# Kernel optimization log

Measured on AMD Instinct MI355X. Metric: run time of the kernel, lower is better.

The kernel has to match this reference:

```python
import jax, jax.numpy as jnp
import numpy as np

N = 200000
E = 6400000


def setup_inputs() -> dict:
    key = jax.random.key(0)
    k1, k2, k3, k4 = jax.random.split(key, 4)
    x = jax.random.normal(k1, (N, 10), dtype=jnp.float32)
    edge_index = jax.random.randint(k2, (2, E), 0, N, dtype=jnp.int64)
    W1 = jax.random.normal(k3, (10, 16), dtype=jnp.float32) * (1.0 / np.sqrt(10))
    b1 = jnp.zeros((16,), dtype=jnp.float32)
    W2 = jax.random.normal(k4, (16, 2), dtype=jnp.float32) * (1.0 / np.sqrt(16))
    b2 = jnp.zeros((2,), dtype=jnp.float32)
    return {"x": x, "edge_index": edge_index, "W1": W1, "b1": b1, "W2": W2, "b2": b2}


def gcn_layer(x, src, dst, W, b, num_nodes):
    # GCNConv: out = D^{-1/2} (A + I) D^{-1/2} (x W) + b, deg computed on A+I
    loop = jnp.arange(num_nodes, dtype=src.dtype)
    s = jnp.concatenate([src, loop])
    d = jnp.concatenate([dst, loop])
    deg = jax.ops.segment_sum(jnp.ones(s.shape[0], dtype=x.dtype), d, num_segments=num_nodes)
    dinv = jnp.where(deg > 0, jax.lax.rsqrt(deg), 0.0)
    norm = dinv[s] * dinv[d]                      # [E+N]
    h = x @ W                                     # [N, out] (transform before gather)
    msg = h[s] * norm[:, None]                    # [E+N, out]
    return jax.ops.segment_sum(msg, d, num_segments=num_nodes) + b


def reference(x, edge_index, W1, b1, W2, b2):
    src, dst = edge_index[0], edge_index[1]
    n = x.shape[0]
    h = jax.nn.relu(gcn_layer(x, src, dst, W1, b1, n))
    return gcn_layer(h, src, dst, W2, b2, n)
```

## Files before the change

### kernel.cpp

```cpp
#include <hip/hip_runtime.h>
#include <hip/hip_fp16.h>

#define BLK 256
#define BBLK 512
#define ABLK 512
#define DBLK 512
#define NBK 782
#define BW 256
#define NK2 512
#define NPAD (NBK * BW)
#define HALF (NPAD / 2)
#define CAP 8960
#define NCH 3
#define CHUNK 6144


__global__ void k_hist(const int* __restrict__ dst, int e, int* __restrict__ gcnt,
                       int* __restrict__ blockhist) {
  __shared__ int h[NBK];
  for (int i = threadIdx.x; i < NBK; i += BLK) h[i] = 0;
  __syncthreads();
  int base = blockIdx.x * CHUNK;
  int m = min(CHUNK, e - base);
  int m4 = m >> 2;
  const int4* d4 = (const int4*)(dst + base);
  for (int k = threadIdx.x; k < m4; k += BLK) {
    int4 vv = d4[k];
    atomicAdd(&h[vv.x >> 8], 1);
    atomicAdd(&h[vv.y >> 8], 1);
    atomicAdd(&h[vv.z >> 8], 1);
    atomicAdd(&h[vv.w >> 8], 1);
  }
  for (int k = (m4 << 2) + threadIdx.x; k < m; k += BLK)
    atomicAdd(&h[dst[base + k] >> 8], 1);
  __syncthreads();
  int* row = blockhist + (size_t)blockIdx.x * NBK;
  int sft = (blockIdx.x * 193) % NBK;
  for (int bb = threadIdx.x; bb < NBK; bb += BLK) {
    int b = bb + sft; if (b >= NBK) b -= NBK;
    int c = h[b];
    row[b] = c;
    if (c) atomicAdd(&gcnt[b], c);
  }
}

__global__ void k_scan(const int* __restrict__ gcnt, int* __restrict__ gbase,
                       int* __restrict__ gcur, int e) {
  __shared__ int s[1024];
  int t = threadIdx.x;
  int v = (t < NBK) ? gcnt[t] : 0;
  s[t] = v;
  __syncthreads();
  for (int d = 1; d < 1024; d <<= 1) {
    int u = (t >= d) ? s[t - d] : 0;
    __syncthreads();
    s[t] += u;
    __syncthreads();
  }
  if (t < NBK) { int ex = s[t] - v; gbase[t] = ex; gcur[t] = ex; }
  if (t == 0) gbase[NBK] = e;
}

__global__ void __launch_bounds__(BBLK) k_bin(const int* __restrict__ src,
                                              const int* __restrict__ dst, int e,
                                              int* __restrict__ gcur,
                                              const int* __restrict__ blockhist,
                                              unsigned* __restrict__ binned) {
  __shared__ int lcnt[NBK];
  __shared__ int loff[NBK + 1];
  __shared__ int lbase[NBK];
  __shared__ int part[BBLK];
  __shared__ unsigned sorted[CHUNK];
  __shared__ unsigned short bkt16[CHUNK];
  int t = threadIdx.x;
  int base = blockIdx.x * CHUNK;
  int m = min(CHUNK, e - base);

  const int* row = blockhist + (size_t)blockIdx.x * NBK;
  for (int i = t; i < NBK; i += BBLK) lcnt[i] = row[i];
  __syncthreads();
  int b0 = 2 * t;
  int s0 = (b0 + 0 < NBK) ? lcnt[b0 + 0] : 0;
  int s1 = (b0 + 1 < NBK) ? lcnt[b0 + 1] : 0;
  int tsum = s0 + s1;
  part[t] = tsum;
  __syncthreads();
  for (int d = 1; d < BBLK; d <<= 1) {
    int u = (t >= d) ? part[t - d] : 0;
    __syncthreads();
    part[t] += u;
    __syncthreads();
  }
  int ex = part[t] - tsum;
  if (b0 + 0 < NBK) loff[b0 + 0] = ex;
  if (b0 + 1 < NBK) loff[b0 + 1] = ex + s0;
  if (t == 0) loff[NBK] = m;
  __syncthreads();
  int sft = (blockIdx.x * 193) % NBK;
  for (int bb = t; bb < NBK; bb += BBLK) {
    int b = bb + sft; if (b >= NBK) b -= NBK;
    int c = lcnt[b];
    lbase[b] = c ? atomicAdd(&gcur[b], c) : 0;
  }
  __syncthreads();
  for (int b = t; b < NBK; b += BBLK) lcnt[b] = loff[b];
  __syncthreads();
  for (int k = t; k < m; k += BBLK) {
    int d = dst[base + k];
    int b = d >> 8;
    int dl = d & 255;
    int pos = atomicAdd(&lcnt[b], 1);
    sorted[pos] = (unsigned)src[base + k] | ((unsigned)dl << 18);
    bkt16[pos] = (unsigned short)b;
  }
  __syncthreads();
  for (int i = t; i < m; i += BBLK) {
    int b = bkt16[i];
    binned[lbase[b] + (i - loff[b])] = sorted[i];
  }
}

__global__ void __launch_bounds__(DBLK) k_ldeg_t1(const unsigned* __restrict__ binned,
                                                  const int* __restrict__ gbase,
                                                  const float* __restrict__ x,
                                                  const float* __restrict__ W1,
                                                  int* __restrict__ deg2,
                                                  float* __restrict__ dinv,
                                                  __half* __restrict__ hs1, int n) {
  __shared__ int cnt[2][NK2];
  __shared__ float w[160];
  int t = threadIdx.x;
  cnt[0][t] = 0;
  cnt[1][t] = 0;
  if (t < 160) w[t] = W1[t];
  __syncthreads();
  int b = blockIdx.x;
  int p0 = gbase[b], p1 = gbase[b + 1];
  int h = t >> 8;
#define KEYOF(u) ((int)(((u) >> 18) << 1) | (int)(((u) & 0x3FFFFu) >= HALF))
  int p = p0 + t;
  for (; p + 3 * DBLK < p1; p += 4 * DBLK) {
    unsigned u0 = binned[p];
    unsigned u1 = binned[p + DBLK];
    unsigned u2 = binned[p + 2 * DBLK];
    unsigned u3 = binned[p + 3 * DBLK];
    atomicAdd(&cnt[h][KEYOF(u0)], 1);
    atomicAdd(&cnt[h][KEYOF(u1)], 1);
    atomicAdd(&cnt[h][KEYOF(u2)], 1);
    atomicAdd(&cnt[h][KEYOF(u3)], 1);
  }
  for (; p < p1; p += DBLK) {
    unsigned u = binned[p];
    atomicAdd(&cnt[h][KEYOF(u)], 1);
  }
#undef KEYOF
  __syncthreads();
  deg2[(size_t)b * NK2 + t] = cnt[0][t] + cnt[1][t];
  if (t >= BW) return;
  int v = b * BW + t;
  if (v >= n) return;
  int dg = cnt[0][2 * t] + cnt[0][2 * t + 1] + cnt[1][2 * t] + cnt[1][2 * t + 1];
  float di = rsqrtf((float)dg + 1.0f);
  dinv[v] = di;
  float xi[10];
#pragma unroll
  for (int k = 0; k < 10; k++) xi[k] = x[(size_t)v * 10 + k];
  __half2 hv[8];
#pragma unroll
  for (int j = 0; j < 8; j++) {
    float acc0 = 0.f, acc1 = 0.f;
#pragma unroll
    for (int k = 0; k < 10; k++) {
      acc0 = fmaf(xi[k], w[k * 16 + 2 * j], acc0);
      acc1 = fmaf(xi[k], w[k * 16 + 2 * j + 1], acc1);
    }
    hv[j] = __floats2half2_rn(acc0 * di, acc1 * di);
  }
  float4* o = (float4*)(hs1 + (size_t)v * 16);
  o[0] = *(float4*)&hv[0];
  o[1] = *(float4*)&hv[4];
}

__global__ void __launch_bounds__(ABLK) k_agg1s(unsigned* __restrict__ binned,
                                                const int* __restrict__ gbase,
                                                const int* __restrict__ deg2,
                                                int* __restrict__ doff,
                                                const __half* __restrict__ hs1,
                                                const float* __restrict__ dinv,
                                                const float* __restrict__ b1,
                                                const float* __restrict__ W2,
                                                float* __restrict__ hs2, int n) {
  __shared__ int cnt[NK2];
  __shared__ int off[NK2 + 1];
  __shared__ int sorted[CAP];
  __shared__ float w2[32];
  __shared__ float sb1[16];
  int t = threadIdx.x;
  if (t < 32) w2[t] = W2[t];
  if (t >= 32 && t < 48) sb1[t - 32] = b1[t - 32];
  int bkt = blockIdx.x;
  int p0 = gbase[bkt], p1 = gbase[bkt + 1];
  const bool fast = (p1 - p0) <= CAP;
  const int j = t >> 1;
  const int c = t & 1;
  float acc[8];
#pragma unroll
  for (int q = 0; q < 8; q++) acc[q] = 0.f;

#define ACCR(R) { const __half2* h2_ = (const __half2*)&R; \
    float2 f0_ = __half22float2(h2_[0]); \
    float2 f1_ = __half22float2(h2_[1]); \
    float2 f2_ = __half22float2(h2_[2]); \
    float2 f3_ = __half22float2(h2_[3]); \
    acc[0] += f0_.x; acc[1] += f0_.y; acc[2] += f1_.x; acc[3] += f1_.y; \
    acc[4] += f2_.x; acc[5] += f2_.y; acc[6] += f3_.x; acc[7] += f3_.y; }

  int p = p0;
  int cidx = 0;
  while (p < p1) {
    int m = min(CAP, p1 - p);
    if (fast) {
      cnt[t] = deg2[(size_t)bkt * NK2 + t];
    } else {
      cnt[t] = 0;
      __syncthreads();
      for (int i = t; i < m; i += ABLK) {
        unsigned u = __builtin_nontemporal_load(&binned[p + i]);
        int key = (int)((u >> 18) << 1) | (int)((u & 0x3FFFFu) >= HALF);
        atomicAdd(&cnt[key], 1);
      }
    }
    __syncthreads();
    int myv = cnt[t];
    for (int d = 1; d < NK2; d <<= 1) {
      int u = (t >= d) ? cnt[t - d] : 0;
      __syncthreads();
      cnt[t] += u;
      __syncthreads();
    }
    off[t] = cnt[t] - myv;
    if (t == 0) off[NK2] = m;
    __syncthreads();
    cnt[t] = off[t];
    __syncthreads();
    for (int i = t; i < m; i += ABLK) {
      unsigned pk = __builtin_nontemporal_load(&binned[p + i]);
      int srcv = (int)(pk & 0x3FFFFu);
      int key = (int)((pk >> 18) << 1) | (int)(srcv >= HALF);
      int pos = atomicAdd(&cnt[key], 1);
      sorted[pos] = srcv;
    }
    __syncthreads();
    for (int i = t; i < m; i += ABLK)
      __builtin_nontemporal_store((unsigned)sorted[i], &binned[p + i]);
    if (cidx < NCH && t <= BW) doff[((size_t)bkt * NCH + cidx) * (BW + 1) + t] = off[2 * t];
    int iA0 = off[2 * j], iA1 = off[2 * j + 1], iB1 = off[2 * j + 2];
    int i = iA0;
    for (; i + 3 < iA1; i += 4) {
      int s0 = sorted[i + 0];
      int s1 = sorted[i + 1];
      int s2 = sorted[i + 2];
      int s3 = sorted[i + 3];
      float4 r0 = *(const float4*)(hs1 + (size_t)s0 * 16 + c * 8);
      float4 r1 = *(const float4*)(hs1 + (size_t)s1 * 16 + c * 8);
      float4 r2 = *(const float4*)(hs1 + (size_t)s2 * 16 + c * 8);
      float4 r3 = *(const float4*)(hs1 + (size_t)s3 * 16 + c * 8);
      ACCR(r0); ACCR(r1); ACCR(r2); ACCR(r3);
    }
    for (; i < iA1; i++) {
      float4 r = *(const float4*)(hs1 + (size_t)sorted[i] * 16 + c * 8);
      ACCR(r);
    }
    __syncthreads();
    for (; i + 3 < iB1; i += 4) {
      int s0 = sorted[i + 0];
      int s1 = sorted[i + 1];
      int s2 = sorted[i + 2];
      int s3 = sorted[i + 3];
      float4 r0 = *(const float4*)(hs1 + (size_t)s0 * 16 + c * 8);
      float4 r1 = *(const float4*)(hs1 + (size_t)s1 * 16 + c * 8);
      float4 r2 = *(const float4*)(hs1 + (size_t)s2 * 16 + c * 8);
      float4 r3 = *(const float4*)(hs1 + (size_t)s3 * 16 + c * 8);
      ACCR(r0); ACCR(r1); ACCR(r2); ACCR(r3);
    }
    for (; i < iB1; i++) {
      float4 r = *(const float4*)(hs1 + (size_t)sorted[i] * 16 + c * 8);
      ACCR(r);
    }
    __syncthreads();
    p += m;
    cidx++;
  }
#undef ACCR

  int v = bkt * BW + j;
  if (v < n) {
    float di = dinv[v];
    float4 sf = *(const float4*)(hs1 + (size_t)v * 16 + c * 8);
    const __half2* sh = (const __half2*)&sf;
    float h0c = 0.f, h1c = 0.f;
#pragma unroll
    for (int q = 0; q < 4; q++) {
      float2 sv = __half22float2(sh[q]);
      int f0 = c * 8 + 2 * q;
      int f1 = f0 + 1;
      float a0 = fmaxf(fmaf(di, acc[2 * q + 0] + sv.x, sb1[f0]), 0.f);
      float a1 = fmaxf(fmaf(di, acc[2 * q + 1] + sv.y, sb1[f1]), 0.f);
      h0c = fmaf(a0, w2[f0 * 2 + 0], fmaf(a1, w2[f1 * 2 + 0], h0c));
      h1c = fmaf(a0, w2[f0 * 2 + 1], fmaf(a1, w2[f1 * 2 + 1], h1c));
    }
    float h0 = h0c + __shfl_xor(h0c, 1);
    float h1 = h1c + __shfl_xor(h1c, 1);
    if (c == 0) {
      hs2[(size_t)v * 2 + 0] = h0 * di;
      hs2[(size_t)v * 2 + 1] = h1 * di;
    }
  }
}

__global__ void __launch_bounds__(BBLK) k_agg2(const unsigned* __restrict__ binned,
                                               const int* __restrict__ gbase,
                                               const int* __restrict__ doff,
                                               const float* __restrict__ hs2,
                                               const float* __restrict__ dinv,
                                               const float* __restrict__ b2,
                                               float* __restrict__ out, int n) {
  int t = threadIdx.x;
  int bkt = blockIdx.x >> 1;
  int j = (t >> 2) + ((blockIdx.x & 1) << 7);
  int c = t & 3;
  int p0 = gbase[bkt], p1 = gbase[bkt + 1];
  float a0 = 0.f, a1 = 0.f;
  int cidx = 0;
  for (int p = p0; p < p1; p += CAP, cidx++) {
    const int* row = doff + ((size_t)bkt * NCH + cidx) * (BW + 1);
    int i0 = row[j], i1 = row[j + 1];
    const unsigned* bp = binned + p;
    int i = i0 + c;
    for (; i + 12 < i1; i += 16) {
      int s0 = bp[i + 0];
      int s1 = bp[i + 4];
      int s2 = bp[i + 8];
      int s3 = bp[i + 12];
      float2 m0 = *(const float2*)(hs2 + (size_t)s0 * 2);
      float2 m1 = *(const float2*)(hs2 + (size_t)s1 * 2);
      float2 m2 = *(const float2*)(hs2 + (size_t)s2 * 2);
      float2 m3 = *(const float2*)(hs2 + (size_t)s3 * 2);
      a0 += m0.x + m1.x + m2.x + m3.x;
      a1 += m0.y + m1.y + m2.y + m3.y;
    }
    for (; i < i1; i += 4) {
      float2 m = *(const float2*)(hs2 + (size_t)bp[i] * 2);
      a0 += m.x;
      a1 += m.y;
    }
  }
  a0 += __shfl_xor(a0, 1);
  a0 += __shfl_xor(a0, 2);
  a1 += __shfl_xor(a1, 1);
  a1 += __shfl_xor(a1, 2);
  int v = bkt * BW + j;
  if (c == 0 && v < n) {
    float di = dinv[v];
    out[(size_t)v * 2 + 0] = fmaf(di, a0 + hs2[(size_t)v * 2 + 0], b2[0]);
    out[(size_t)v * 2 + 1] = fmaf(di, a1 + hs2[(size_t)v * 2 + 1], b2[1]);
  }
}

extern "C" void kernel_launch(void* const* d_in, const int* in_sizes, int n_in,
                              void* d_out, int out_size, void* d_ws, size_t ws_size,
                              hipStream_t stream) {
  const float* x  = (const float*)d_in[0];
  const int*   ei = (const int*)d_in[1];
  const float* W1 = (const float*)d_in[2];
  const float* b1 = (const float*)d_in[3];
  const float* W2 = (const float*)d_in[4];
  const float* b2 = (const float*)d_in[5];
  float* out = (float*)d_out;

  const int n = in_sizes[0] / 10;
  const int e = in_sizes[1] / 2;
  const int* src = ei;
  const int* dst = ei + e;

  int gC = (e + CHUNK - 1) / CHUNK;

  char* ws = (char*)d_ws;
  int*      gcnt      = (int*)ws;      ws += (size_t)NBK * 4;
  int*      gbase     = (int*)ws;      ws += ((size_t)NBK + 1) * 4;
  int*      gcur      = (int*)ws;      ws += (size_t)NBK * 4;
  int*      deg2      = (int*)ws;      ws += (size_t)NBK * NK2 * 4;
  int*      doff      = (int*)ws;      ws += (size_t)NBK * NCH * (BW + 1) * 4;
  int*      blockhist = (int*)ws;      ws += (size_t)gC * NBK * 4;
  unsigned* binned    = (unsigned*)ws; ws += (size_t)e * 4;
  float*    dinv      = (float*)ws;    ws += (size_t)n * 4;
  __half*   hs1       = (__half*)ws;   ws += (size_t)NPAD * 16 * 2;
  float*    hs2       = (float*)ws;    ws += (size_t)n * 2 * 4;

  hipMemsetAsync(gcnt, 0, (size_t)NBK * 4, stream);
  k_hist<<<gC, BLK, 0, stream>>>(dst, e, gcnt, blockhist);
  k_scan<<<1, 1024, 0, stream>>>(gcnt, gbase, gcur, e);
  k_bin<<<gC, BBLK, 0, stream>>>(src, dst, e, gcur, blockhist, binned);
  k_ldeg_t1<<<NBK, DBLK, 0, stream>>>(binned, gbase, x, W1, deg2, dinv, hs1, n);
  k_agg1s<<<NBK, ABLK, 0, stream>>>(binned, gbase, deg2, doff, hs1, dinv, b1, W2, hs2, n);
  k_agg2<<<NBK * 2, BBLK, 0, stream>>>(binned, gbase, doff, hs2, dinv, b2, out, n);
}
```

Before: 298.8 us.

## Balance layer-1 gather by splitting edge ranges evenly across threads

The layer-1 aggregation used to give each destination node's thread pair exactly its own edges, so per-thread work followed the node degree. It now reorders the sort key so all low-half sources come first, then splits each half's edge range evenly across thread pairs. Each thread run-length accumulates per destination and flushes to a shared-memory accumulator with atomics. The second-layer kernel and the offset table are updated for the new key layout, and CAP shrinks to make room for the shared accumulator, at the cost of extra LDS atomics and per-edge destination checks.

```diff
diff --git a/kernel.cpp b/kernel.cpp
--- a/kernel.cpp
+++ b/kernel.cpp
@@ -10,7 +10,7 @@
 #define NK2 512
 #define NPAD (NBK * BW)
 #define HALF (NPAD / 2)
-#define CAP 8960
+#define CAP 8640
 #define NCH 3
 #define CHUNK 6144
 
@@ -137,7 +137,7 @@
   int b = blockIdx.x;
   int p0 = gbase[b], p1 = gbase[b + 1];
   int h = t >> 8;
-#define KEYOF(u) ((int)(((u) >> 18) << 1) | (int)(((u) & 0x3FFFFu) >= HALF))
+#define KEYOF(u) ((int)((u) >> 18) | ((((u) & 0x3FFFFu) >= (unsigned)HALF) ? 256 : 0))
   int p = p0 + t;
   for (; p + 3 * DBLK < p1; p += 4 * DBLK) {
     unsigned u0 = binned[p];
@@ -159,7 +159,7 @@
   if (t >= BW) return;
   int v = b * BW + t;
   if (v >= n) return;
-  int dg = cnt[0][2 * t] + cnt[0][2 * t + 1] + cnt[1][2 * t] + cnt[1][2 * t + 1];
+  int dg = cnt[0][t] + cnt[1][t] + cnt[0][256 + t] + cnt[1][256 + t];
   float di = rsqrtf((float)dg + 1.0f);
   dinv[v] = di;
   float xi[10];
@@ -191,29 +191,75 @@
                                                 const float* __restrict__ W2,
                                                 float* __restrict__ hs2, int n) {
   __shared__ int cnt[NK2];
-  __shared__ int off[NK2 + 1];
   __shared__ int sorted[CAP];
+  __shared__ float accL[BW][16];
   __shared__ float w2[32];
   __shared__ float sb1[16];
+  __shared__ int shmA;
   int t = threadIdx.x;
   if (t < 32) w2[t] = W2[t];
   if (t >= 32 && t < 48) sb1[t - 32] = b1[t - 32];
+  {
+    float* az = &accL[0][0];
+    for (int i = t; i < BW * 16; i += ABLK) az[i] = 0.f;
+  }
   int bkt = blockIdx.x;
   int p0 = gbase[bkt], p1 = gbase[bkt + 1];
   const bool fast = (p1 - p0) <= CAP;
   const int j = t >> 1;
   const int c = t & 1;
-  float acc[8];
-#pragma unroll
-  for (int q = 0; q < 8; q++) acc[q] = 0.f;
-
-#define ACCR(R) { const __half2* h2_ = (const __half2*)&R; \
-    float2 f0_ = __half22float2(h2_[0]); \
-    float2 f1_ = __half22float2(h2_[1]); \
-    float2 f2_ = __half22float2(h2_[2]); \
-    float2 f3_ = __half22float2(h2_[3]); \
-    acc[0] += f0_.x; acc[1] += f0_.y; acc[2] += f1_.x; acc[3] += f1_.y; \
-    acc[4] += f2_.x; acc[5] += f2_.y; acc[6] += f3_.x; acc[7] += f3_.y; }
+  const int c8 = c * 8;
+
+  float aa[8] = {0.f, 0.f, 0.f, 0.f, 0.f, 0.f, 0.f, 0.f};
+  int cdl = -1;
+  auto flush = [&]() {
+    if (cdl >= 0) {
+#pragma unroll
+      for (int f = 0; f < 8; f++) atomicAdd(&accL[cdl][c8 + f], aa[f]);
+    }
+  };
+  auto step = [&](int sv, float4 R) {
+    int dl_ = sv >> 18;
+    if (dl_ != cdl) {
+      flush();
+      cdl = dl_;
+#pragma unroll
+      for (int f = 0; f < 8; f++) aa[f] = 0.f;
+    }
+    const __half2* h2_ = (const __half2*)&R;
+    float2 f0_ = __half22float2(h2_[0]);
+    float2 f1_ = __half22float2(h2_[1]);
+    float2 f2_ = __half22float2(h2_[2]);
+    float2 f3_ = __half22float2(h2_[3]);
+    aa[0] += f0_.x; aa[1] += f0_.y; aa[2] += f1_.x; aa[3] += f1_.y;
+    aa[4] += f2_.x; aa[5] += f2_.y; aa[6] += f3_.x; aa[7] += f3_.y;
+  };
+  auto gatherRange = [&](int lo, int hi) {
+    int tot = hi - lo;
+    if (tot <= 0) return;
+    int cs = (tot + BW - 1) >> 8;
+    int i0 = lo + j * cs;
+    int i1 = min(hi, i0 + cs);
+    cdl = -1;
+    int i = i0;
+    for (; i + 3 < i1; i += 4) {
+      int s0 = sorted[i + 0];
+      int s1 = sorted[i + 1];
+      int s2 = sorted[i + 2];
+      int s3 = sorted[i + 3];
+      float4 r0 = *(const float4*)(hs1 + (size_t)(s0 & 0x3FFFF) * 16 + c8);
+      float4 r1 = *(const float4*)(hs1 + (size_t)(s1 & 0x3FFFF) * 16 + c8);
+      float4 r2 = *(const float4*)(hs1 + (size_t)(s2 & 0x3FFFF) * 16 + c8);
+      float4 r3 = *(const float4*)(hs1 + (size_t)(s3 & 0x3FFFF) * 16 + c8);
+      step(s0, r0); step(s1, r1); step(s2, r2); step(s3, r3);
+    }
+    for (; i < i1; i++) {
+      int s = sorted[i];
+      float4 r = *(const float4*)(hs1 + (size_t)(s & 0x3FFFF) * 16 + c8);
+      step(s, r);
+    }
+    flush();
+  };
 
   int p = p0;
   int cidx = 0;
@@ -226,7 +272,7 @@
       __syncthreads();
       for (int i = t; i < m; i += ABLK) {
         unsigned u = __builtin_nontemporal_load(&binned[p + i]);
-        int key = (int)((u >> 18) << 1) | (int)((u & 0x3FFFFu) >= HALF);
+        int key = (int)(u >> 18) | (((u & 0x3FFFFu) >= (unsigned)HALF) ? 256 : 0);
         atomicAdd(&cnt[key], 1);
       }
     }
@@ -238,74 +284,46 @@
       cnt[t] += u;
       __syncthreads();
     }
-    off[t] = cnt[t] - myv;
-    if (t == 0) off[NK2] = m;
-    __syncthreads();
-    cnt[t] = off[t];
+    if (t == 255) shmA = cnt[255];
+    int ex = cnt[t] - myv;
+    cnt[t] = ex;
+    if (cidx < NCH) {
+      int* drow = doff + ((size_t)bkt * NCH + cidx) * (NK2 + 1);
+      drow[t] = ex;
+      if (t == NK2 - 1) drow[NK2] = m;
+    }
     __syncthreads();
     for (int i = t; i < m; i += ABLK) {
       unsigned pk = __builtin_nontemporal_load(&binned[p + i]);
-      int srcv = (int)(pk & 0x3FFFFu);
-      int key = (int)((pk >> 18) << 1) | (int)(srcv >= HALF);
+      int key = (int)(pk >> 18) | (((pk & 0x3FFFFu) >= (unsigned)HALF) ? 256 : 0);
       int pos = atomicAdd(&cnt[key], 1);
-      sorted[pos] = srcv;
+      sorted[pos] = (int)pk;
     }
     __syncthreads();
     for (int i = t; i < m; i += ABLK)
-      __builtin_nontemporal_store((unsigned)sorted[i], &binned[p + i]);
-    if (cidx < NCH && t <= BW) doff[((size_t)bkt * NCH + cidx) * (BW + 1) + t] = off[2 * t];
-    int iA0 = off[2 * j], iA1 = off[2 * j + 1], iB1 = off[2 * j + 2];
-    int i = iA0;
-    for (; i + 3 < iA1; i += 4) {
-      int s0 = sorted[i + 0];
-      int s1 = sorted[i + 1];
-      int s2 = sorted[i + 2];
-      int s3 = sorted[i + 3];
-      float4 r0 = *(const float4*)(hs1 + (size_t)s0 * 16 + c * 8);
-      float4 r1 = *(const float4*)(hs1 + (size_t)s1 * 16 + c * 8);
-      float4 r2 = *(const float4*)(hs1 + (size_t)s2 * 16 + c * 8);
-      float4 r3 = *(const float4*)(hs1 + (size_t)s3 * 16 + c * 8);
-      ACCR(r0); ACCR(r1); ACCR(r2); ACCR(r3);
-    }
-    for (; i < iA1; i++) {
-      float4 r = *(const float4*)(hs1 + (size_t)sorted[i] * 16 + c * 8);
-      ACCR(r);
-    }
-    __syncthreads();
-    for (; i + 3 < iB1; i += 4) {
-      int s0 = sorted[i + 0];
-      int s1 = sorted[i + 1];
-      int s2 = sorted[i + 2];
-      int s3 = sorted[i + 3];
-      float4 r0 = *(const float4*)(hs1 + (size_t)s0 * 16 + c * 8);
-      float4 r1 = *(const float4*)(hs1 + (size_t)s1 * 16 + c * 8);
-      float4 r2 = *(const float4*)(hs1 + (size_t)s2 * 16 + c * 8);
-      float4 r3 = *(const float4*)(hs1 + (size_t)s3 * 16 + c * 8);
-      ACCR(r0); ACCR(r1); ACCR(r2); ACCR(r3);
-    }
-    for (; i < iB1; i++) {
-      float4 r = *(const float4*)(hs1 + (size_t)sorted[i] * 16 + c * 8);
-      ACCR(r);
-    }
+      __builtin_nontemporal_store((unsigned)(sorted[i] & 0x3FFFF), &binned[p + i]);
+    int mA = shmA;
+    gatherRange(0, mA);
+    __syncthreads();
+    gatherRange(mA, m);
     __syncthreads();
     p += m;
     cidx++;
   }
-#undef ACCR
 
   int v = bkt * BW + j;
   if (v < n) {
     float di = dinv[v];
-    float4 sf = *(const float4*)(hs1 + (size_t)v * 16 + c * 8);
+    float4 sf = *(const float4*)(hs1 + (size_t)v * 16 + c8);
     const __half2* sh = (const __half2*)&sf;
     float h0c = 0.f, h1c = 0.f;
 #pragma unroll
     for (int q = 0; q < 4; q++) {
       float2 sv = __half22float2(sh[q]);
-      int f0 = c * 8 + 2 * q;
+      int f0 = c8 + 2 * q;
       int f1 = f0 + 1;
-      float a0 = fmaxf(fmaf(di, acc[2 * q + 0] + sv.x, sb1[f0]), 0.f);
-      float a1 = fmaxf(fmaf(di, acc[2 * q + 1] + sv.y, sb1[f1]), 0.f);
+      float a0 = fmaxf(fmaf(di, accL[j][f0] + sv.x, sb1[f0]), 0.f);
+      float a1 = fmaxf(fmaf(di, accL[j][f1] + sv.y, sb1[f1]), 0.f);
       h0c = fmaf(a0, w2[f0 * 2 + 0], fmaf(a1, w2[f1 * 2 + 0], h0c));
       h1c = fmaf(a0, w2[f0 * 2 + 1], fmaf(a1, w2[f1 * 2 + 1], h1c));
     }
@@ -333,26 +351,29 @@
   float a0 = 0.f, a1 = 0.f;
   int cidx = 0;
   for (int p = p0; p < p1; p += CAP, cidx++) {
-    const int* row = doff + ((size_t)bkt * NCH + cidx) * (BW + 1);
-    int i0 = row[j], i1 = row[j + 1];
+    const int* row = doff + ((size_t)bkt * NCH + cidx) * (NK2 + 1);
     const unsigned* bp = binned + p;
-    int i = i0 + c;
-    for (; i + 12 < i1; i += 16) {
-      int s0 = bp[i + 0];
-      int s1 = bp[i + 4];
-      int s2 = bp[i + 8];
-      int s3 = bp[i + 12];
-      float2 m0 = *(const float2*)(hs2 + (size_t)s0 * 2);
-      float2 m1 = *(const float2*)(hs2 + (size_t)s1 * 2);
-      float2 m2 = *(const float2*)(hs2 + (size_t)s2 * 2);
-      float2 m3 = *(const float2*)(hs2 + (size_t)s3 * 2);
-      a0 += m0.x + m1.x + m2.x + m3.x;
-      a1 += m0.y + m1.y + m2.y + m3.y;
-    }
-    for (; i < i1; i += 4) {
-      float2 m = *(const float2*)(hs2 + (size_t)bp[i] * 2);
-      a0 += m.x;
-      a1 += m.y;
+#pragma unroll
+    for (int seg = 0; seg < 2; seg++) {
+      int i0 = row[(seg << 8) + j], i1 = row[(seg << 8) + j + 1];
+      int i = i0 + c;
+      for (; i + 12 < i1; i += 16) {
+        int s0 = bp[i + 0];
+        int s1 = bp[i + 4];
+        int s2 = bp[i + 8];
+        int s3 = bp[i + 12];
+        float2 m0 = *(const float2*)(hs2 + (size_t)s0 * 2);
+        float2 m1 = *(const float2*)(hs2 + (size_t)s1 * 2);
+        float2 m2 = *(const float2*)(hs2 + (size_t)s2 * 2);
+        float2 m3 = *(const float2*)(hs2 + (size_t)s3 * 2);
+        a0 += m0.x + m1.x + m2.x + m3.x;
+        a1 += m0.y + m1.y + m2.y + m3.y;
+      }
+      for (; i < i1; i += 4) {
+        float2 m = *(const float2*)(hs2 + (size_t)bp[i] * 2);
+        a0 += m.x;
+        a1 += m.y;
+      }
     }
   }
   a0 += __shfl_xor(a0, 1);
@@ -390,7 +411,7 @@
   int*      gbase     = (int*)ws;      ws += ((size_t)NBK + 1) * 4;
   int*      gcur      = (int*)ws;      ws += (size_t)NBK * 4;
   int*      deg2      = (int*)ws;      ws += (size_t)NBK * NK2 * 4;
-  int*      doff      = (int*)ws;      ws += (size_t)NBK * NCH * (BW + 1) * 4;
+  int*      doff      = (int*)ws;      ws += (size_t)NBK * NCH * (NK2 + 1) * 4;
   int*      blockhist = (int*)ws;      ws += (size_t)gC * NBK * 4;
   unsigned* binned    = (unsigned*)ws; ws += (size_t)e * 4;
   float*    dinv      = (float*)ws;    ws += (size_t)n * 4;
```

Result: slower. 334.3 us (+11.9%).
